# Performance work log

Hardware: AMD Instinct MI355X
Metric: run time of the kernel (lower is better)

## Reference

```python
import jax, jax.numpy as jnp
import numpy as np

D_MODEL = 1024
N_HEADS = 16
D_HEAD = D_MODEL // N_HEADS
B, S = 4, 2048


def setup_inputs() -> dict:
    key = jax.random.key(0)
    ks = jax.random.split(key, 9)
    s = 1.0 / np.sqrt(D_MODEL)
    inp = {
        "x": jax.random.normal(ks[0], (B, S, D_MODEL), dtype=jnp.float32),
        "W_q": jax.random.uniform(ks[1], (D_MODEL, D_MODEL), jnp.float32, -s, s),
        "b_q": jax.random.uniform(ks[2], (D_MODEL,), jnp.float32, -s, s),
        "W_k": jax.random.uniform(ks[3], (D_MODEL, D_MODEL), jnp.float32, -s, s),
        "b_k": jax.random.uniform(ks[4], (D_MODEL,), jnp.float32, -s, s),
        "W_v": jax.random.uniform(ks[5], (D_MODEL, D_MODEL), jnp.float32, -s, s),
        "b_v": jax.random.uniform(ks[6], (D_MODEL,), jnp.float32, -s, s),
        "W_o": jax.random.uniform(ks[7], (D_MODEL, D_MODEL), jnp.float32, -s, s),
        "b_o": jax.random.uniform(ks[8], (D_MODEL,), jnp.float32, -s, s),
    }
    return inp


def reference(x, W_q, b_q, W_k, b_k, W_v, b_v, W_o, b_o):
    b, s, d = x.shape
    # Project and split heads: [b, h, s, d_head]
    def split(t):
        return t.reshape(b, s, N_HEADS, D_HEAD).transpose(0, 2, 1, 3)
    Q = split(x @ W_q + b_q)
    K = split(x @ W_k + b_k)
    V = split(x @ W_v + b_v)
    scores = jnp.einsum('bhqd,bhkd->bhqk', Q, K) / np.sqrt(D_HEAD).astype(np.float32)
    causal = jnp.triu(jnp.full((s, s), -jnp.inf, dtype=scores.dtype), k=1)
    scores = scores + causal
    attn = jax.nn.softmax(scores, axis=-1)  # dropout p=0 -> identity
    ctx = jnp.einsum('bhqk,bhkd->bhqd', attn, V)
    ctx = ctx.transpose(0, 2, 1, 3).reshape(b, s, d)
    return ctx @ W_o + b_o
```

## Files before the change

### kernel.cpp

```cpp
#include <hip/hip_runtime.h>
#include <stdint.h>

#define B_    4
#define S_    2048
#define DM    1024
#define NH    16
#define DH    64
#define BH    (B_ * NH)
#define MROWS (B_ * S_)
#define LOG2E 1.4426950408889634f

typedef __attribute__((ext_vector_type(8))) short short8;
typedef __attribute__((ext_vector_type(4))) float f32x4;
typedef __attribute__((ext_vector_type(16))) float f32x16;
typedef __attribute__((ext_vector_type(4))) unsigned int u32x4;

__device__ __forceinline__ unsigned short f2bf(float f) {
  unsigned int u = __float_as_uint(f);
  u = (u + 0x7FFFu + ((u >> 16) & 1u)) >> 16;
  return (unsigned short)u;
}
__device__ __forceinline__ unsigned int pack_bf16(float lo, float hi) {
  unsigned int a = (__float_as_uint(lo) + 0x8000u) >> 16;
  unsigned int b = (__float_as_uint(hi) + 0x8000u) & 0xFFFF0000u;
  return a | b;
}

__device__ __forceinline__ void gll16(const void* g, const void* l) {
  __builtin_amdgcn_global_load_lds(
      (__attribute__((address_space(1))) void*)(unsigned long long)g,
      (__attribute__((address_space(3))) void*)(unsigned int)(unsigned long long)l,
      16, 0, 0);
}

__global__ __launch_bounds__(256) void prep_kernel(
    const float* __restrict__ x,
    const float* __restrict__ Wq, const float* __restrict__ Wk,
    const float* __restrict__ Wv, const float* __restrict__ Wo,
    unsigned short* __restrict__ xb,
    unsigned short* __restrict__ wt_qkv, unsigned short* __restrict__ wt_o) {
  __shared__ float t[32][33];
  const int z = blockIdx.z;
  if (z >= 4) {
    size_t lb = (size_t)(z - 4) * 1024 + blockIdx.y * 32 + blockIdx.x;
    size_t i = (lb * 256 + threadIdx.x) * 8;
    float4 a = *(const float4*)(x + i);
    float4 b = *(const float4*)(x + i + 4);
    short8 o;
    o[0] = (short)f2bf(a.x); o[1] = (short)f2bf(a.y);
    o[2] = (short)f2bf(a.z); o[3] = (short)f2bf(a.w);
    o[4] = (short)f2bf(b.x); o[5] = (short)f2bf(b.y);
    o[6] = (short)f2bf(b.z); o[7] = (short)f2bf(b.w);
    *(short8*)(xb + i) = o;
    return;
  }
  const float* W = z == 0 ? Wq : z == 1 ? Wk : z == 2 ? Wv : Wo;
  unsigned short* dst = z < 3 ? wt_qkv + (size_t)z * DM * DM : wt_o;
  const int nb = blockIdx.x * 32, kb = blockIdx.y * 32;
  const int tx = threadIdx.x & 31, ty = threadIdx.x >> 5;
#pragma unroll
  for (int p = 0; p < 4; ++p) {
    int r = ty + p * 8;
    t[r][tx] = W[(size_t)(kb + r) * DM + nb + tx];
  }
  __syncthreads();
#pragma unroll
  for (int p = 0; p < 4; ++p) {
    int r = ty + p * 8;
    dst[(size_t)(nb + r) * DM + kb + tx] = f2bf(t[tx][r]);
  }
}

__device__ __forceinline__ void gemm_core(const unsigned short* __restrict__ A,
                                          const unsigned short* __restrict__ Bt,
                                          int m0, int n0,
                                          unsigned short* As, unsigned short* Bs,
                                          f32x16 (&acc)[2][2]) {
  const int tid = threadIdx.x;
  const int lane = tid & 63, wave = tid >> 6;
  const int l31 = lane & 31, half = lane >> 5;
  const int wm = (wave >> 1) * 64, wn = (wave & 1) * 64;

  for (int kk = 0; kk < DM; kk += 64) {
#pragma unroll
    for (int p = 0; p < 4; ++p) {
      int idx = p * 256 + tid;
      int row = idx >> 3, ch = idx & 7;
      int sc = (ch ^ (row & 7)) << 3;
      gll16(A  + (size_t)(m0 + row) * DM + kk + sc, As + idx * 8);
      gll16(Bt + (size_t)(n0 + row) * DM + kk + sc, Bs + idx * 8);
    }
    __syncthreads();
#pragma unroll
    for (int ks = 0; ks < 4; ++ks) {
      short8 af[2], bf[2];
#pragma unroll
      for (int mi = 0; mi < 2; ++mi) {
        int row = wm + mi * 32 + l31;
        af[mi] = *(const short8*)&As[row * 64 + (((ks * 2 + half) ^ (l31 & 7)) << 3)];
      }
#pragma unroll
      for (int nj = 0; nj < 2; ++nj) {
        int row = wn + nj * 32 + l31;
        bf[nj] = *(const short8*)&Bs[row * 64 + (((ks * 2 + half) ^ (l31 & 7)) << 3)];
      }
#pragma unroll
      for (int mi = 0; mi < 2; ++mi)
#pragma unroll
        for (int nj = 0; nj < 2; ++nj)
          acc[mi][nj] = __builtin_amdgcn_mfma_f32_32x32x16_bf16(af[mi], bf[nj], acc[mi][nj], 0, 0, 0);
    }
    __syncthreads();
  }
}

__global__ __launch_bounds__(256) void gemm_qkv_kernel(
    const unsigned short* __restrict__ xb, const unsigned short* __restrict__ wt,
    const float* __restrict__ bq, const float* __restrict__ bk, const float* __restrict__ bv,
    unsigned short* __restrict__ Qb, unsigned short* __restrict__ Kb,
    unsigned short* __restrict__ Vt) {
  __shared__ unsigned short As[128 * 64];
  __shared__ unsigned short Bs[128 * 64];
  f32x16 acc[2][2] = {};
  const int m0 = blockIdx.y * 128, n0 = blockIdx.x * 128;
  gemm_core(xb, wt, m0, n0, As, Bs, acc);

  const int tid = threadIdx.x, lane = tid & 63, wave = tid >> 6;
  const int l31 = lane & 31, half = lane >> 5;
  const int wm = (wave >> 1) * 64, wn = (wave & 1) * 64;
  const int which = n0 >> 10;
  const int nb = n0 - (which << 10);
  if (which == 2) {
#pragma unroll
    for (int nj = 0; nj < 2; ++nj) {
      int n10 = nb + wn + nj * 32 + l31;
      float bsv = bv[n10];
      int h = n10 >> 6, d = n10 & 63;
#pragma unroll
      for (int mi = 0; mi < 2; ++mi) {
#pragma unroll
        for (int reg = 0; reg < 16; ++reg) {
          int m = m0 + wm + mi * 32 + (reg & 3) + 8 * (reg >> 2) + 4 * half;
          int b = m >> 11, s = m & 2047;
          Vt[(((size_t)(b * NH + h)) * DH + d) * S_ + s] = f2bf(acc[mi][nj][reg] + bsv);
        }
      }
    }
    return;
  }
  const float* bias = which == 0 ? bq : bk;
  unsigned short* dst = which == 0 ? Qb : Kb;
  const float scale = (which == 0) ? 0.125f * LOG2E : 1.0f;
#pragma unroll
  for (int nj = 0; nj < 2; ++nj) {
    int n10 = nb + wn + nj * 32 + l31;
    float bsv = bias[n10];
    int h = n10 >> 6, d = n10 & 63;
#pragma unroll
    for (int mi = 0; mi < 2; ++mi) {
#pragma unroll
      for (int reg = 0; reg < 16; ++reg) {
        int m = m0 + wm + mi * 32 + (reg & 3) + 8 * (reg >> 2) + 4 * half;
        int b = m >> 11, s = m & 2047;
        float v = (acc[mi][nj][reg] + bsv) * scale;
        dst[(((size_t)(b * NH + h)) * S_ + s) * DH + d] = f2bf(v);
      }
    }
  }
}

__global__ __launch_bounds__(256) void gemm_out_kernel(
    const unsigned short* __restrict__ ctx, const unsigned short* __restrict__ wto,
    const float* __restrict__ bo, float* __restrict__ out) {
  __shared__ unsigned short As[128 * 64];
  __shared__ unsigned short Bs[128 * 64];
  f32x16 acc[2][2] = {};
  const int m0 = blockIdx.y * 128, n0 = blockIdx.x * 128;
  gemm_core(ctx, wto, m0, n0, As, Bs, acc);

  const int tid = threadIdx.x, lane = tid & 63, wave = tid >> 6;
  const int l31 = lane & 31, half = lane >> 5;
  const int wm = (wave >> 1) * 64, wn = (wave & 1) * 64;
#pragma unroll
  for (int nj = 0; nj < 2; ++nj) {
    int n = n0 + wn + nj * 32 + l31;
    float bsv = bo[n];
#pragma unroll
    for (int mi = 0; mi < 2; ++mi) {
#pragma unroll
      for (int reg = 0; reg < 16; ++reg) {
        int m = m0 + wm + mi * 32 + (reg & 3) + 8 * (reg >> 2) + 4 * half;
        out[(size_t)m * DM + n] = acc[mi][nj][reg] + bsv;
      }
    }
  }
}

__global__ __launch_bounds__(256, 3) void attn_kernel(
    const unsigned short* __restrict__ Qb, const unsigned short* __restrict__ Kb,
    const unsigned short* __restrict__ Vt, unsigned short* __restrict__ ctx) {
  __shared__ unsigned short Ks[128 * 64];
  __shared__ unsigned short Vs[64 * 128];

  const int tid = threadIdx.x, lane = tid & 63, wave = tid >> 6;
  const int col = lane & 15, quad = lane >> 4;
  const int bh = blockIdx.x;
  const int qt = 15 - blockIdx.y;
  const int b = bh >> 4, h = bh & 15;

  const unsigned short* Qp = Qb + ((size_t)bh * S_ + qt * 128) * DH;
  const unsigned short* Kbase = Kb + (size_t)bh * S_ * DH;
  const unsigned short* Vbase = Vt + (size_t)bh * DH * S_;

#pragma unroll
  for (int p = 0; p < 4; ++p) {
    int idx = p * 256 + tid;
    int row = idx >> 3, ch = idx & 7;
    int sc = (ch ^ (row & 7)) << 3;
    gll16(Kbase + row * 64 + sc, Ks + idx * 8);
  }
  short8 qf[2][2];
#pragma unroll
  for (int i = 0; i < 2; ++i)
#pragma unroll
    for (int ksd = 0; ksd < 2; ++ksd)
      qf[i][ksd] = *(const short8*)(Qp + (wave * 32 + i * 16 + col) * 64 + ksd * 32 + quad * 8);
  __syncthreads();

  f32x4 o[2][4] = {};
  f32x4 lacc[2] = {};

  const int idxA = (col + ((lane & 16) << 1)) << 2;
  const int idxB = idxA + 64;
  const bool hij = (lane & 32) != 0;

  for (int kt = 0; kt <= qt; ++kt) {
    const unsigned short* Vp = Vbase + kt * 128;
#pragma unroll
    for (int p = 0; p < 4; ++p) {
      int idx = p * 256 + tid;
      int row = idx >> 4, ch = idx & 15;
      int sc = (ch & 8) | ((ch ^ row) & 7);
      gll16(Vp + (size_t)row * S_ + sc * 8, Vs + idx * 8);
    }

    f32x4 sa[2][8];
#pragma unroll
    for (int jt = 0; jt < 8; ++jt) {
      int row = jt * 16 + col;
      short8 kf0 = *(const short8*)&Ks[row * 64 + ((quad ^ (row & 7)) << 3)];
      short8 kf1 = *(const short8*)&Ks[row * 64 + (((4 + quad) ^ (row & 7)) << 3)];
#pragma unroll
      for (int i = 0; i < 2; ++i) {
        f32x4 c = {-8.f, -8.f, -8.f, -8.f};
        c = __builtin_amdgcn_mfma_f32_16x16x32_bf16(kf0, qf[i][0], c, 0, 0, 0);
        c = __builtin_amdgcn_mfma_f32_16x16x32_bf16(kf1, qf[i][1], c, 0, 0, 0);
        sa[i][jt] = c;
      }
    }

    if (kt == qt) {
#pragma unroll
      for (int i = 0; i < 2; ++i) {
        int ql = wave * 32 + i * 16 + col;
#pragma unroll
        for (int jt = 0; jt < 8; ++jt)
#pragma unroll
          for (int r = 0; r < 4; ++r)
            if (jt * 16 + quad * 4 + r > ql) sa[i][jt][r] = -__builtin_inff();
      }
    }

    unsigned int ppk[2][8][2];
#pragma unroll
    for (int i = 0; i < 2; ++i)
#pragma unroll
      for (int jt = 0; jt < 8; ++jt) {
        f32x4 p;
#pragma unroll
        for (int c4 = 0; c4 < 4; ++c4) {
          p[c4] = __builtin_amdgcn_exp2f(sa[i][jt][c4]);
          lacc[i][c4] += p[c4];
        }
        ppk[i][jt][0] = pack_bf16(p[0], p[1]);
        ppk[i][jt][1] = pack_bf16(p[2], p[3]);
      }

    __syncthreads();

    if (kt < qt) {
      const unsigned short* Kp = Kbase + (size_t)(kt + 1) * 128 * DH;
#pragma unroll
      for (int p = 0; p < 4; ++p) {
        int idx = p * 256 + tid;
        int row = idx >> 3, ch = idx & 7;
        int sc = (ch ^ (row & 7)) << 3;
        gll16(Kp + row * 64 + sc, Ks + idx * 8);
      }
    }

#pragma unroll
    for (int ks = 0; ks < 4; ++ks) {
      short8 vf[4];
#pragma unroll
      for (int jo = 0; jo < 4; ++jo) {
        int row = jo * 16 + col;
        int c = ks * 4 + quad;
        int ch = (c & 8) | ((c ^ row) & 7);
        vf[jo] = *(const short8*)&Vs[row * 128 + ch * 8];
      }
#pragma unroll
      for (int i = 0; i < 2; ++i) {
        int p0 = (int)ppk[i][2 * ks][0], p1 = (int)ppk[i][2 * ks][1];
        int q0 = (int)ppk[i][2 * ks + 1][0], q1 = (int)ppk[i][2 * ks + 1][1];
        int a0 = __builtin_amdgcn_ds_bpermute(idxA, p0);
        int b0 = __builtin_amdgcn_ds_bpermute(idxA, q0);
        int a1 = __builtin_amdgcn_ds_bpermute(idxA, p1);
        int b1 = __builtin_amdgcn_ds_bpermute(idxA, q1);
        int a2 = __builtin_amdgcn_ds_bpermute(idxB, p0);
        int b2 = __builtin_amdgcn_ds_bpermute(idxB, q0);
        int a3 = __builtin_amdgcn_ds_bpermute(idxB, p1);
        int b3 = __builtin_amdgcn_ds_bpermute(idxB, q1);
        u32x4 uu;
        uu[0] = (unsigned)(hij ? b0 : a0);
        uu[1] = (unsigned)(hij ? b1 : a1);
        uu[2] = (unsigned)(hij ? b2 : a2);
        uu[3] = (unsigned)(hij ? b3 : a3);
        short8 af = __builtin_bit_cast(short8, uu);
#pragma unroll
        for (int jo = 0; jo < 4; ++jo)
          o[i][jo] = __builtin_amdgcn_mfma_f32_16x16x32_bf16(af, vf[jo], o[i][jo], 0, 0, 0);
      }
    }
    __syncthreads();
  }

#pragma unroll
  for (int i = 0; i < 2; ++i) {
    float l = (lacc[i][0] + lacc[i][1]) + (lacc[i][2] + lacc[i][3]);
    l += __shfl_xor(l, 16);
    l += __shfl_xor(l, 32);
#pragma unroll
    for (int r = 0; r < 4; ++r) {
      float lr = __shfl(l, ((lane >> 4) << 2) + r);
      float inv = __builtin_amdgcn_rcpf(lr);
      int s = qt * 128 + wave * 32 + i * 16 + quad * 4 + r;
#pragma unroll
      for (int jo = 0; jo < 4; ++jo) {
        int d = jo * 16 + col;
        ctx[((size_t)(b * S_ + s)) * DM + h * DH + d] = f2bf(o[i][jo][r] * inv);
      }
    }
  }
}

extern "C" void kernel_launch(void* const* d_in, const int* in_sizes, int n_in,
                              void* d_out, int out_size, void* d_ws, size_t ws_size,
                              hipStream_t stream) {
  (void)in_sizes; (void)n_in; (void)out_size; (void)ws_size;
  const float* x  = (const float*)d_in[0];
  const float* Wq = (const float*)d_in[1];
  const float* bq = (const float*)d_in[2];
  const float* Wk = (const float*)d_in[3];
  const float* bk = (const float*)d_in[4];
  const float* Wv = (const float*)d_in[5];
  const float* bv = (const float*)d_in[6];
  const float* Wo = (const float*)d_in[7];
  const float* bo = (const float*)d_in[8];
  float* out = (float*)d_out;

  char* ws = (char*)d_ws;
  size_t off = 0;
  auto carve = [&](size_t bytes) -> char* {
    char* p = ws + off;
    off += (bytes + 255) & ~(size_t)255;
    return p;
  };
  unsigned short* xb  = (unsigned short*)carve((size_t)MROWS * DM * 2);
  unsigned short* wtq = (unsigned short*)carve((size_t)3 * DM * DM * 2);
  unsigned short* wto = (unsigned short*)carve((size_t)DM * DM * 2);
  unsigned short* Qb  = (unsigned short*)carve((size_t)BH * S_ * DH * 2);
  unsigned short* Kb  = (unsigned short*)carve((size_t)BH * S_ * DH * 2);
  unsigned short* Vt  = (unsigned short*)carve((size_t)BH * S_ * DH * 2);
  unsigned short* ctx = (unsigned short*)carve((size_t)BH * S_ * DH * 2);

  prep_kernel<<<dim3(32, 32, 8), 256, 0, stream>>>(x, Wq, Wk, Wv, Wo, xb, wtq, wto);
  gemm_qkv_kernel<<<dim3(24, 64), 256, 0, stream>>>(xb, wtq, bq, bk, bv, Qb, Kb, Vt);
  attn_kernel<<<dim3(64, 16), 256, 0, stream>>>(Qb, Kb, Vt, ctx);
  gemm_out_kernel<<<dim3(8, 64), 256, 0, stream>>>(ctx, wto, bo, out);
}
```

Measured before the change: 265.2 us.

## Switch attention kernel MFMAs from 16x16x32 to 32x32x16 tiles

Result: slower. 377.1 us (+42.2%).

```diff
diff --git a/kernel.cpp b/kernel.cpp
--- a/kernel.cpp
+++ b/kernel.cpp
@@ -203,7 +203,7 @@
   __shared__ unsigned short Vs[64 * 128];
 
   const int tid = threadIdx.x, lane = tid & 63, wave = tid >> 6;
-  const int col = lane & 15, quad = lane >> 4;
+  const int l31 = lane & 31, half = lane >> 5;
   const int bh = blockIdx.x;
   const int qt = 15 - blockIdx.y;
   const int b = bh >> 4, h = bh & 15;
@@ -219,20 +219,14 @@
     int sc = (ch ^ (row & 7)) << 3;
     gll16(Kbase + row * 64 + sc, Ks + idx * 8);
   }
-  short8 qf[2][2];
-#pragma unroll
-  for (int i = 0; i < 2; ++i)
-#pragma unroll
-    for (int ksd = 0; ksd < 2; ++ksd)
-      qf[i][ksd] = *(const short8*)(Qp + (wave * 32 + i * 16 + col) * 64 + ksd * 32 + quad * 8);
+  short8 qf[4];
+#pragma unroll
+  for (int ks = 0; ks < 4; ++ks)
+    qf[ks] = *(const short8*)(Qp + (wave * 32 + l31) * 64 + ks * 16 + half * 8);
   __syncthreads();
 
-  f32x4 o[2][4] = {};
-  f32x4 lacc[2] = {};
-
-  const int idxA = (col + ((lane & 16) << 1)) << 2;
-  const int idxB = idxA + 64;
-  const bool hij = (lane & 32) != 0;
+  f32x16 o[2] = {};
+  f32x4 lacc = {};
 
   for (int kt = 0; kt <= qt; ++kt) {
     const unsigned short* Vp = Vbase + kt * 128;
@@ -244,47 +238,61 @@
       gll16(Vp + (size_t)row * S_ + sc * 8, Vs + idx * 8);
     }
 
-    f32x4 sa[2][8];
-#pragma unroll
-    for (int jt = 0; jt < 8; ++jt) {
-      int row = jt * 16 + col;
-      short8 kf0 = *(const short8*)&Ks[row * 64 + ((quad ^ (row & 7)) << 3)];
-      short8 kf1 = *(const short8*)&Ks[row * 64 + (((4 + quad) ^ (row & 7)) << 3)];
-#pragma unroll
-      for (int i = 0; i < 2; ++i) {
-        f32x4 c = {-8.f, -8.f, -8.f, -8.f};
-        c = __builtin_amdgcn_mfma_f32_16x16x32_bf16(kf0, qf[i][0], c, 0, 0, 0);
-        c = __builtin_amdgcn_mfma_f32_16x16x32_bf16(kf1, qf[i][1], c, 0, 0, 0);
-        sa[i][jt] = c;
-      }
-    }
-
-    if (kt == qt) {
-#pragma unroll
-      for (int i = 0; i < 2; ++i) {
-        int ql = wave * 32 + i * 16 + col;
-#pragma unroll
-        for (int jt = 0; jt < 8; ++jt)
-#pragma unroll
-          for (int r = 0; r < 4; ++r)
-            if (jt * 16 + quad * 4 + r > ql) sa[i][jt][r] = -__builtin_inff();
-      }
-    }
-
-    unsigned int ppk[2][8][2];
-#pragma unroll
-    for (int i = 0; i < 2; ++i)
-#pragma unroll
-      for (int jt = 0; jt < 8; ++jt) {
-        f32x4 p;
-#pragma unroll
-        for (int c4 = 0; c4 < 4; ++c4) {
-          p[c4] = __builtin_amdgcn_exp2f(sa[i][jt][c4]);
-          lacc[i][c4] += p[c4];
+    short8 pa[8];
+#pragma unroll
+    for (int t = 0; t < 4; ++t) {
+      f32x16 sa;
+#pragma unroll
+      for (int r = 0; r < 16; ++r) sa[r] = -8.f;
+      int row = t * 32 + l31;
+#pragma unroll
+      for (int ks = 0; ks < 4; ++ks) {
+        short8 kf = *(const short8*)&Ks[row * 64 + (((ks * 2 + half) ^ (row & 7)) << 3)];
+        sa = __builtin_amdgcn_mfma_f32_32x32x16_bf16(kf, qf[ks], sa, 0, 0, 0);
+      }
+      if (kt == qt) {
+        int ql = wave * 32 + l31;
+#pragma unroll
+        for (int r = 0; r < 16; ++r) {
+          int kv = t * 32 + (r & 3) + 8 * (r >> 2) + 4 * half;
+          if (kv > ql) sa[r] = -__builtin_inff();
         }
-        ppk[i][jt][0] = pack_bf16(p[0], p[1]);
-        ppk[i][jt][1] = pack_bf16(p[2], p[3]);
-      }
+      }
+      float p[16];
+#pragma unroll
+      for (int r = 0; r < 16; ++r) {
+        p[r] = __builtin_amdgcn_exp2f(sa[r]);
+        lacc[r & 3] += p[r];
+      }
+      {
+        unsigned int A0 = pack_bf16(p[0], p[1]), A1 = pack_bf16(p[2], p[3]);
+        unsigned int B0 = pack_bf16(p[4], p[5]), B1 = pack_bf16(p[6], p[7]);
+        unsigned int A0x = (unsigned int)__shfl_xor((int)A0, 32);
+        unsigned int A1x = (unsigned int)__shfl_xor((int)A1, 32);
+        unsigned int B0x = (unsigned int)__shfl_xor((int)B0, 32);
+        unsigned int B1x = (unsigned int)__shfl_xor((int)B1, 32);
+        u32x4 fa;
+        fa[0] = half ? B0x : A0;
+        fa[1] = half ? B1x : A1;
+        fa[2] = half ? B0  : A0x;
+        fa[3] = half ? B1  : A1x;
+        pa[2 * t] = __builtin_bit_cast(short8, fa);
+      }
+      {
+        unsigned int C0 = pack_bf16(p[8], p[9]),   C1 = pack_bf16(p[10], p[11]);
+        unsigned int D0 = pack_bf16(p[12], p[13]), D1 = pack_bf16(p[14], p[15]);
+        unsigned int C0x = (unsigned int)__shfl_xor((int)C0, 32);
+        unsigned int C1x = (unsigned int)__shfl_xor((int)C1, 32);
+        unsigned int D0x = (unsigned int)__shfl_xor((int)D0, 32);
+        unsigned int D1x = (unsigned int)__shfl_xor((int)D1, 32);
+        u32x4 fb;
+        fb[0] = half ? D0x : C0;
+        fb[1] = half ? D1x : C1;
+        fb[2] = half ? D0  : C0x;
+        fb[3] = half ? D1  : C1x;
+        pa[2 * t + 1] = __builtin_bit_cast(short8, fb);
+      }
+    }
 
     __syncthreads();
 
@@ -300,56 +308,30 @@
     }
 
 #pragma unroll
-    for (int ks = 0; ks < 4; ++ks) {
-      short8 vf[4];
-#pragma unroll
-      for (int jo = 0; jo < 4; ++jo) {
-        int row = jo * 16 + col;
-        int c = ks * 4 + quad;
-        int ch = (c & 8) | ((c ^ row) & 7);
-        vf[jo] = *(const short8*)&Vs[row * 128 + ch * 8];
-      }
-#pragma unroll
-      for (int i = 0; i < 2; ++i) {
-        int p0 = (int)ppk[i][2 * ks][0], p1 = (int)ppk[i][2 * ks][1];
-        int q0 = (int)ppk[i][2 * ks + 1][0], q1 = (int)ppk[i][2 * ks + 1][1];
-        int a0 = __builtin_amdgcn_ds_bpermute(idxA, p0);
-        int b0 = __builtin_amdgcn_ds_bpermute(idxA, q0);
-        int a1 = __builtin_amdgcn_ds_bpermute(idxA, p1);
-        int b1 = __builtin_amdgcn_ds_bpermute(idxA, q1);
-        int a2 = __builtin_amdgcn_ds_bpermute(idxB, p0);
-        int b2 = __builtin_amdgcn_ds_bpermute(idxB, q0);
-        int a3 = __builtin_amdgcn_ds_bpermute(idxB, p1);
-        int b3 = __builtin_amdgcn_ds_bpermute(idxB, q1);
-        u32x4 uu;
-        uu[0] = (unsigned)(hij ? b0 : a0);
-        uu[1] = (unsigned)(hij ? b1 : a1);
-        uu[2] = (unsigned)(hij ? b2 : a2);
-        uu[3] = (unsigned)(hij ? b3 : a3);
-        short8 af = __builtin_bit_cast(short8, uu);
-#pragma unroll
-        for (int jo = 0; jo < 4; ++jo)
-          o[i][jo] = __builtin_amdgcn_mfma_f32_16x16x32_bf16(af, vf[jo], o[i][jo], 0, 0, 0);
+    for (int s2 = 0; s2 < 8; ++s2) {
+#pragma unroll
+      for (int jd = 0; jd < 2; ++jd) {
+        int row = jd * 32 + l31;
+        int c = s2 * 2 + half;
+        short8 vf = *(const short8*)&Vs[row * 128 + (((c & 8) | ((c ^ row) & 7)) << 3)];
+        o[jd] = __builtin_amdgcn_mfma_f32_32x32x16_bf16(pa[s2], vf, o[jd], 0, 0, 0);
       }
     }
     __syncthreads();
   }
 
-#pragma unroll
-  for (int i = 0; i < 2; ++i) {
-    float l = (lacc[i][0] + lacc[i][1]) + (lacc[i][2] + lacc[i][3]);
-    l += __shfl_xor(l, 16);
-    l += __shfl_xor(l, 32);
-#pragma unroll
-    for (int r = 0; r < 4; ++r) {
-      float lr = __shfl(l, ((lane >> 4) << 2) + r);
-      float inv = __builtin_amdgcn_rcpf(lr);
-      int s = qt * 128 + wave * 32 + i * 16 + quad * 4 + r;
-#pragma unroll
-      for (int jo = 0; jo < 4; ++jo) {
-        int d = jo * 16 + col;
-        ctx[((size_t)(b * S_ + s)) * DM + h * DH + d] = f2bf(o[i][jo][r] * inv);
-      }
+  float l = (lacc[0] + lacc[1]) + (lacc[2] + lacc[3]);
+  l += __shfl_xor(l, 32);
+#pragma unroll
+  for (int r = 0; r < 16; ++r) {
+    int qrow = (r & 3) + 8 * (r >> 2) + 4 * half;
+    float lr = __shfl(l, qrow);
+    float inv = __builtin_amdgcn_rcpf(lr);
+    int s = qt * 128 + wave * 32 + qrow;
+#pragma unroll
+    for (int jd = 0; jd < 2; ++jd) {
+      int d = jd * 32 + l31;
+      ctx[((size_t)(b * S_ + s)) * DM + h * DH + d] = f2bf(o[jd][r] * inv);
     }
   }
 }
```
